# Kernel tuning notes

Hardware: AMD Instinct MI355X
Metric: run time of the kernel (lower is better)

The kernel has to match this reference:

```python
import jax, jax.numpy as jnp
import numpy as np

H = 1536
NH = 24
HD = 64
B = 2
S = 2048


def _rotate_half(x):
    x1, x2 = x[..., : HD // 2], x[..., HD // 2 :]
    return jnp.concatenate((-x2, x1), axis=-1)


def setup_inputs() -> dict:
    key = jax.random.key(0)
    ks = jax.random.split(key, 8)
    scale = 1.0 / np.sqrt(H)
    pos = jnp.arange(S)[:, None]
    inv_freq = 1.0 / (10000.0 ** (jnp.arange(0, HD, 2, dtype=jnp.float32) / HD))
    ang = pos * inv_freq[None, :]
    ang = jnp.concatenate([ang, ang], axis=-1)  # [S, HD]
    return {
        "hidden_states": jax.random.normal(ks[0], (B, S, H), jnp.float32),
        "rope_cos": jnp.cos(ang),
        "rope_sin": jnp.sin(ang),
        "wq": jax.random.normal(ks[1], (H, H), jnp.float32) * scale,
        "bq": jnp.zeros((H,), jnp.float32),
        "wk": jax.random.normal(ks[2], (H, H), jnp.float32) * scale,
        "bk": jnp.zeros((H,), jnp.float32),
        "wv": jax.random.normal(ks[3], (H, H), jnp.float32) * scale,
        "bv": jnp.zeros((H,), jnp.float32),
        "wo": jax.random.normal(ks[4], (H, H), jnp.float32) * scale,
        "bo": jnp.zeros((H,), jnp.float32),
    }


def reference(hidden_states, rope_cos, rope_sin, wq, bq, wk, bk, wv, bv, wo, bo):
    b, s, _ = hidden_states.shape
    # QKV projections (torch Linear: x @ W.T + b)
    q = hidden_states @ wq.T + bq
    k = hidden_states @ wk.T + bk
    v = hidden_states @ wv.T + bv
    # [B, NH, S, HD]
    q = q.reshape(b, s, NH, HD).transpose(0, 2, 1, 3)
    k = k.reshape(b, s, NH, HD).transpose(0, 2, 1, 3)
    v = v.reshape(b, s, NH, HD).transpose(0, 2, 1, 3)
    # RoPE: cos/sin broadcast over batch & heads
    cos = rope_cos[None, None, :, :]
    sin = rope_sin[None, None, :, :]
    q = q * cos + _rotate_half(q) * sin
    k = k * cos + _rotate_half(k) * sin
    # SDPA
    scores = jnp.einsum("bhqd,bhkd->bhqk", q, k) / jnp.sqrt(jnp.float32(HD))
    attn = jax.nn.softmax(scores, axis=-1)
    out = jnp.einsum("bhqk,bhkd->bhqd", attn, v)
    out = out.transpose(0, 2, 1, 3).reshape(b, s, NH * HD)
    return out @ wo.T + bo
```

## Files before the change

### kernel.cpp

```cpp
#include <hip/hip_runtime.h>
#include <hip/hip_bf16.h>
#include <cstdint>

namespace {
constexpr int H_  = 1536;
constexpr int NH_ = 24;
constexpr int HD_ = 64;
constexpr int B_  = 2;
constexpr int S_  = 2048;
constexpr int M_  = B_ * S_;
constexpr int KD_ = H_;
}

typedef __attribute__((ext_vector_type(8))) short  bf16x8;
typedef __attribute__((ext_vector_type(4))) float  f32x4;

__device__ __forceinline__ unsigned short f2bf_fast(float x) {
    return (unsigned short)((__float_as_uint(x) + 0x8000u) >> 16);
}
__device__ __forceinline__ unsigned pack2bf(float b_hi, float a_lo) {
    const unsigned ub = __float_as_uint(b_hi) + 0x8000u;
    const unsigned ua = __float_as_uint(a_lo) + 0x8000u;
    return (ub & 0xffff0000u) | (ua >> 16);
}

__device__ __forceinline__ void gload16(const short* g, short* l) {
    __builtin_amdgcn_global_load_lds(
        (const __attribute__((address_space(1))) unsigned int*)g,
        (__attribute__((address_space(3))) unsigned int*)l, 16, 0, 0);
}

__global__ __launch_bounds__(256)
void cast_all(const float* __restrict__ X,
              const float* __restrict__ wq, const float* __restrict__ wk,
              const float* __restrict__ wv, const float* __restrict__ wo,
              short* __restrict__ Xh,
              short* __restrict__ Wqh, short* __restrict__ Wkh,
              short* __restrict__ Wvh, short* __restrict__ Woh)
{
    constexpr int XB = (M_*H_) / 1024;
    constexpr int WB = (H_*H_) / 1024;
    const int bid = blockIdx.x;
    const float* src; short* dst; int off;
    if (bid < XB)            { src = X;  dst = Xh;  off = bid; }
    else {
        const int r = bid - XB, wsel = r / WB; off = r % WB;
        if      (wsel == 0)  { src = wq; dst = Wqh; }
        else if (wsel == 1)  { src = wk; dst = Wkh; }
        else if (wsel == 2)  { src = wv; dst = Wvh; }
        else                 { src = wo; dst = Woh; }
    }
    const int i = (off * 256 + threadIdx.x) * 4;
    const float4 v = *(const float4*)&src[i];
    uint2 o;
    o.x = pack2bf(v.y, v.x);
    o.y = pack2bf(v.w, v.z);
    *(uint2*)&dst[i] = o;
}

template<int KIND>
__global__ __launch_bounds__(256, 4)
void gemm_bf16(const short* __restrict__ A_g,
               const short* __restrict__ Wq, const short* __restrict__ Wk,
               const short* __restrict__ Wv,
               const float* __restrict__ bq, const float* __restrict__ bk,
               const float* __restrict__ bv,
               const float* __restrict__ cosb, const float* __restrict__ sinb,
               short* __restrict__ Qb, short* __restrict__ Kb,
               short* __restrict__ Vt, float* __restrict__ outf)
{
    __shared__ short Ah[128*64], Bh[128*64];

    const int t    = threadIdx.x;
    const int lane = t & 63;
    const int w    = t >> 6;
    const int wr   = w >> 1, wc = w & 1;
    const int l15  = lane & 15;
    const int grp  = lane >> 4;

    const int xcd = blockIdx.x & 7;
    const int off = blockIdx.x >> 3;
    const int m_idx = xcd * 4 + (off & 3);
    const int rest  = off >> 2;
    const int n_idx = rest % 12;
    const int zi    = (KIND == 0) ? rest / 12 : 3;

    const int m0 = m_idx * 128;
    const int n0 = n_idx * 128;

    const short* bhg; const float* bias;
    if (KIND == 0) {
        if      (zi == 0) { bhg = Wq; bias = bq; }
        else if (zi == 1) { bhg = Wk; bias = bk; }
        else              { bhg = Wv; bias = bv; }
    } else {
        bhg = Wq; bias = bq;
    }

    f32x4 acc[4][4];
#pragma unroll
    for (int i = 0; i < 4; ++i)
#pragma unroll
        for (int j = 0; j < 4; ++j) acc[i][j] = (f32x4){0.f, 0.f, 0.f, 0.f};

    const int srow  = lane >> 3;
    const int sslot = (lane & 7) ^ srow;

    for (int kt = 0; kt < KD_; kt += 64) {
        __syncthreads();
#pragma unroll
        for (int cc = 0; cc < 4; ++cc) {
            const int c = w * 4 + cc;
            const int r = c * 8 + srow;
            gload16(A_g + (size_t)(m0 + r) * KD_ + kt + sslot * 8, Ah + c * 512);
            gload16(bhg + (size_t)(n0 + r) * KD_ + kt + sslot * 8, Bh + c * 512);
        }
        __syncthreads();

#pragma unroll
        for (int kk = 0; kk < 2; ++kk) {
            bf16x8 af[4], bfr[4];
#pragma unroll
            for (int i = 0; i < 4; ++i) {
                const int ra = wr * 64 + i * 16 + l15;
                af[i]  = *(const bf16x8*)&Ah[ra * 64 + (((kk*4 + grp) ^ (ra & 7)) << 3)];
                const int rb = wc * 64 + i * 16 + l15;
                bfr[i] = *(const bf16x8*)&Bh[rb * 64 + (((kk*4 + grp) ^ (rb & 7)) << 3)];
            }
#pragma unroll
            for (int i = 0; i < 4; ++i)
#pragma unroll
                for (int j = 0; j < 4; ++j)
                    acc[i][j] = __builtin_amdgcn_mfma_f32_16x16x32_bf16(af[i], bfr[j], acc[i][j], 0, 0, 0);
        }
    }

    float bn[4];
#pragma unroll
    for (int ni = 0; ni < 4; ++ni) bn[ni] = bias[n0 + wc * 64 + ni * 16 + l15];
    const int hw = (n0 + wc * 64) >> 6;

    if (KIND == 1) {
#pragma unroll
        for (int mi = 0; mi < 4; ++mi)
#pragma unroll
            for (int r = 0; r < 4; ++r) {
                const int m = m0 + wr * 64 + mi * 16 + grp * 4 + r;
#pragma unroll
                for (int ni = 0; ni < 4; ++ni)
                    outf[(size_t)m * H_ + n0 + wc * 64 + ni * 16 + l15] =
                        acc[mi][ni][r] + bn[ni];
            }
        return;
    }

    if (zi == 2) {
        const int b = m0 >> 11;
#pragma unroll
        for (int mi = 0; mi < 4; ++mi) {
            const int sb = (m0 & (S_ - 1)) + wr * 64 + mi * 16 + grp * 4;
#pragma unroll
            for (int ni = 0; ni < 4; ++ni) {
                const int d = ni * 16 + l15;
                uint2 o;
                o.x = pack2bf(acc[mi][ni][1] + bn[ni], acc[mi][ni][0] + bn[ni]);
                o.y = pack2bf(acc[mi][ni][3] + bn[ni], acc[mi][ni][2] + bn[ni]);
                *(uint2*)&Vt[((size_t)(b * NH_ + hw) * HD_ + d) * S_ + sb] = o;
            }
        }
        return;
    }

    const float sc = (zi == 0) ? 0.18033688011112042f : 1.0f;
    short* dst = (zi == 0) ? Qb : Kb;
#pragma unroll
    for (int mi = 0; mi < 4; ++mi)
#pragma unroll
        for (int r = 0; r < 4; ++r) {
            const int m = m0 + wr * 64 + mi * 16 + grp * 4 + r;
            const int b = m >> 11;
            const int s = m & (S_ - 1);
#pragma unroll
            for (int ni = 0; ni < 4; ++ni) {
                const int d  = ni * 16 + l15;
                const float val = acc[mi][ni][r] + bn[ni];
                const float pv  = acc[mi][ni ^ 2][r] + bn[ni ^ 2];
                const float cs = cosb[s * HD_ + d];
                const float sn = sinb[s * HD_ + d];
                const float rot = (ni < 2) ? -pv : pv;
                dst[((size_t)(b * NH_ + hw) * S_ + s) * HD_ + d] =
                    (short)f2bf_fast((val * cs + rot * sn) * sc);
            }
        }
}

__global__ __launch_bounds__(256)
void attn_mfma(const short* __restrict__ Q, const short* __restrict__ K,
               const short* __restrict__ Vt, short* __restrict__ AO)
{
    __shared__ short Ks[2][4096];
    __shared__ short Vs[2][4096];
    __shared__ short Ps[4][1024];

    const int t    = threadIdx.x;
    const int lane = t & 63;
    const int wid  = t >> 6;
    const int bh   = blockIdx.y;
    const int q0   = blockIdx.x * 64;

    const int l15 = lane & 15;
    const int grp = lane >> 4;
    const int sw  = lane & 7;

    const short* Qg = Q  + ((size_t)bh * S_ + q0 + wid*16) * HD_;
    const short* Kg = K  + (size_t)bh * S_ * HD_;
    const short* Vg = Vt + (size_t)bh * HD_ * S_;

    bf16x8 qf[2];
#pragma unroll
    for (int f = 0; f < 2; ++f)
        qf[f] = *(const bf16x8*)(Qg + (size_t)l15*HD_ + f*32 + grp*8);

    f32x4 oacc[4];
#pragma unroll
    for (int nt = 0; nt < 4; ++nt) oacc[nt] = (f32x4){0.f,0.f,0.f,0.f};
    float lacc = 0.f;

    auto stageKV = [&](int b, int kt) {
#pragma unroll
        for (int cc = 0; cc < 2; ++cc) {
            const int d   = cc * 256 + t;
            const int row = d >> 3;
            const int sg  = (d & 7) ^ (row & 7);
            gload16(Kg + (size_t)(kt + row) * HD_ + sg * 8, &Ks[b][d * 8]);
            gload16(Vg + (size_t)row * S_ + kt + sg * 8,    &Vs[b][d * 8]);
        }
    };

    stageKV(0, 0);
    __syncthreads();
    int cur = 0;

    for (int kt = 0; kt < S_; kt += 64) {
        if (kt + 64 < S_) stageKV(cur ^ 1, kt + 64);

        f32x4 sac[4];
#pragma unroll
        for (int nt = 0; nt < 4; ++nt) sac[nt] = (f32x4){0.f,0.f,0.f,0.f};
        __builtin_amdgcn_s_setprio(1);
#pragma unroll
        for (int f = 0; f < 2; ++f) {
            const int slotf = ((grp + f*4) ^ sw) << 3;
#pragma unroll
            for (int nt = 0; nt < 4; ++nt) {
                const bf16x8 kfrag = *(const bf16x8*)&Ks[cur][(nt*16 + l15)*64 + slotf];
                sac[nt] = __builtin_amdgcn_mfma_f32_16x16x32_bf16(kfrag, qf[f], sac[nt], 0, 0, 0);
            }
        }
        __builtin_amdgcn_s_setprio(0);

#pragma unroll
        for (int nt = 0; nt < 4; ++nt)
#pragma unroll
            for (int r = 0; r < 4; ++r) {
                sac[nt][r] = exp2f(sac[nt][r]);
                lacc += sac[nt][r];
            }

#pragma unroll
        for (int nt = 0; nt < 4; ++nt)
#pragma unroll
            for (int rp = 0; rp < 2; ++rp) {
                const int kv0 = nt*16 + grp*4 + rp*2;
                const int idx = l15*64 + (((kv0 >> 3) ^ sw) << 3) + (kv0 & 7);
                *(unsigned*)&Ps[wid][idx] =
                    pack2bf(sac[nt][rp*2+1], sac[nt][rp*2]);
            }

        __builtin_amdgcn_s_setprio(1);
#pragma unroll
        for (int f = 0; f < 2; ++f) {
            const int slotf = ((grp + f*4) ^ sw) << 3;
            const bf16x8 pfrag = *(const bf16x8*)&Ps[wid][l15*64 + slotf];
#pragma unroll
            for (int nt = 0; nt < 4; ++nt) {
                const bf16x8 vfrag = *(const bf16x8*)&Vs[cur][(nt*16 + l15)*64 + slotf];
                oacc[nt] = __builtin_amdgcn_mfma_f32_16x16x32_bf16(vfrag, pfrag, oacc[nt], 0, 0, 0);
            }
        }
        __builtin_amdgcn_s_setprio(0);

        __syncthreads();
        cur ^= 1;
    }

    lacc += __shfl_xor(lacc, 16);
    lacc += __shfl_xor(lacc, 32);
    const float inv = 1.f / lacc;

    const int b = bh / NH_, h = bh % NH_;
    const int srow = q0 + wid*16 + l15;
    const size_t rowb = ((size_t)(b*S_ + srow)) * H_ + h*HD_;
#pragma unroll
    for (int nt = 0; nt < 4; ++nt) {
        uint2 o;
        o.x = pack2bf(oacc[nt][1]*inv, oacc[nt][0]*inv);
        o.y = pack2bf(oacc[nt][3]*inv, oacc[nt][2]*inv);
        *(uint2*)&AO[rowb + nt*16 + grp*4] = o;
    }
}

extern "C" void kernel_launch(void* const* d_in, const int* in_sizes, int n_in,
                              void* d_out, int out_size, void* d_ws, size_t ws_size,
                              hipStream_t stream)
{
    const float* X    = (const float*)d_in[0];
    const float* cosb = (const float*)d_in[1];
    const float* sinb = (const float*)d_in[2];
    const float* wq   = (const float*)d_in[3];
    const float* bq   = (const float*)d_in[4];
    const float* wk   = (const float*)d_in[5];
    const float* bk   = (const float*)d_in[6];
    const float* wv   = (const float*)d_in[7];
    const float* bv   = (const float*)d_in[8];
    const float* wo   = (const float*)d_in[9];
    const float* bo   = (const float*)d_in[10];
    float* out = (float*)d_out;

    const size_t MH = (size_t)M_ * H_;
    const size_t HH = (size_t)H_ * H_;

    short* Xh  = (short*)d_ws;
    short* Wqh = Xh  + MH;
    short* Wkh = Wqh + HH;
    short* Wvh = Wkh + HH;
    short* Woh = Wvh + HH;
    short* Qb  = Woh + HH;
    short* Kb  = Qb + MH;
    short* Vt  = Kb + MH;
    short* AO  = Vt + MH;

    cast_all<<<(int)(MH/1024 + 4*(HH/1024)), 256, 0, stream>>>(
        X, wq, wk, wv, wo, Xh, Wqh, Wkh, Wvh, Woh);

    gemm_bf16<0><<<1152, 256, 0, stream>>>(Xh, Wqh, Wkh, Wvh,
        bq, bk, bv, cosb, sinb, Qb, Kb, Vt, nullptr);

    attn_mfma<<<dim3(S_/64, B_*NH_), 256, 0, stream>>>(Qb, Kb, Vt, AO);

    gemm_bf16<1><<<384, 256, 0, stream>>>(AO, Woh, nullptr, nullptr,
        bo, nullptr, nullptr, nullptr, nullptr, nullptr, nullptr, nullptr, out);
}
```

Measured before the change: 225.4 us.

## Switch attention to 32x32x16 MFMA with 128-row query tiles per block

The attention kernel now uses 32x32x16 bf16 MFMA, and each wave handles 32 query rows instead of 16, so a block covers 128 queries. Each K/V tile staged in LDS is reused across twice as many queries, which halves global K/V traffic and LDS fragment reads per query row. Launch bounds request 3 blocks per SM. The cost is more registers per wave (16-wide accumulators), a larger P buffer in LDS, half as many blocks (768), and more complex scattered output stores.

```diff
diff --git a/kernel.cpp b/kernel.cpp
--- a/kernel.cpp
+++ b/kernel.cpp
@@ -12,8 +12,9 @@
 constexpr int KD_ = H_;
 }
 
-typedef __attribute__((ext_vector_type(8))) short  bf16x8;
-typedef __attribute__((ext_vector_type(4))) float  f32x4;
+typedef __attribute__((ext_vector_type(8)))  short bf16x8;
+typedef __attribute__((ext_vector_type(4)))  float f32x4;
+typedef __attribute__((ext_vector_type(16))) float f32x16;
 
 __device__ __forceinline__ unsigned short f2bf_fast(float x) {
     return (unsigned short)((__float_as_uint(x) + 0x8000u) >> 16);
@@ -194,36 +195,38 @@
         }
 }
 
-__global__ __launch_bounds__(256)
+__global__ __launch_bounds__(256, 3)
 void attn_mfma(const short* __restrict__ Q, const short* __restrict__ K,
                const short* __restrict__ Vt, short* __restrict__ AO)
 {
     __shared__ short Ks[2][4096];
     __shared__ short Vs[2][4096];
-    __shared__ short Ps[4][1024];
+    __shared__ short Ps[4][2048];
 
     const int t    = threadIdx.x;
     const int lane = t & 63;
     const int wid  = t >> 6;
     const int bh   = blockIdx.y;
-    const int q0   = blockIdx.x * 64;
-
-    const int l15 = lane & 15;
-    const int grp = lane >> 4;
-    const int sw  = lane & 7;
-
-    const short* Qg = Q  + ((size_t)bh * S_ + q0 + wid*16) * HD_;
+    const int q0   = blockIdx.x * 128;
+
+    const int l31 = lane & 31;
+    const int hi  = lane >> 5;
+    const int sw7 = lane & 7;
+
+    const short* Qg = Q  + ((size_t)bh * S_ + q0 + wid*32) * HD_;
     const short* Kg = K  + (size_t)bh * S_ * HD_;
     const short* Vg = Vt + (size_t)bh * HD_ * S_;
 
-    bf16x8 qf[2];
-#pragma unroll
-    for (int f = 0; f < 2; ++f)
-        qf[f] = *(const bf16x8*)(Qg + (size_t)l15*HD_ + f*32 + grp*8);
-
-    f32x4 oacc[4];
-#pragma unroll
-    for (int nt = 0; nt < 4; ++nt) oacc[nt] = (f32x4){0.f,0.f,0.f,0.f};
+    bf16x8 qf[4];
+#pragma unroll
+    for (int kk = 0; kk < 4; ++kk)
+        qf[kk] = *(const bf16x8*)(Qg + (size_t)l31*HD_ + kk*16 + hi*8);
+
+    f32x16 oacc[2];
+#pragma unroll
+    for (int nt = 0; nt < 2; ++nt)
+#pragma unroll
+        for (int r = 0; r < 16; ++r) oacc[nt][r] = 0.f;
     float lacc = 0.f;
 
     auto stageKV = [&](int b, int kt) {
@@ -244,48 +247,53 @@
     for (int kt = 0; kt < S_; kt += 64) {
         if (kt + 64 < S_) stageKV(cur ^ 1, kt + 64);
 
-        f32x4 sac[4];
-#pragma unroll
-        for (int nt = 0; nt < 4; ++nt) sac[nt] = (f32x4){0.f,0.f,0.f,0.f};
+        f32x16 sac[2];
+#pragma unroll
+        for (int nt = 0; nt < 2; ++nt)
+#pragma unroll
+            for (int r = 0; r < 16; ++r) sac[nt][r] = 0.f;
         __builtin_amdgcn_s_setprio(1);
 #pragma unroll
-        for (int f = 0; f < 2; ++f) {
-            const int slotf = ((grp + f*4) ^ sw) << 3;
-#pragma unroll
-            for (int nt = 0; nt < 4; ++nt) {
-                const bf16x8 kfrag = *(const bf16x8*)&Ks[cur][(nt*16 + l15)*64 + slotf];
-                sac[nt] = __builtin_amdgcn_mfma_f32_16x16x32_bf16(kfrag, qf[f], sac[nt], 0, 0, 0);
+        for (int kk = 0; kk < 4; ++kk) {
+#pragma unroll
+            for (int nt = 0; nt < 2; ++nt) {
+                const int row = nt*32 + l31;
+                const bf16x8 kfrag = *(const bf16x8*)
+                    &Ks[cur][row*64 + (((kk*2 + hi) ^ sw7) << 3)];
+                sac[nt] = __builtin_amdgcn_mfma_f32_32x32x16_bf16(kfrag, qf[kk], sac[nt], 0, 0, 0);
             }
         }
         __builtin_amdgcn_s_setprio(0);
 
 #pragma unroll
-        for (int nt = 0; nt < 4; ++nt)
-#pragma unroll
-            for (int r = 0; r < 4; ++r) {
+        for (int nt = 0; nt < 2; ++nt)
+#pragma unroll
+            for (int r = 0; r < 16; ++r) {
                 sac[nt][r] = exp2f(sac[nt][r]);
                 lacc += sac[nt][r];
             }
 
 #pragma unroll
-        for (int nt = 0; nt < 4; ++nt)
-#pragma unroll
-            for (int rp = 0; rp < 2; ++rp) {
-                const int kv0 = nt*16 + grp*4 + rp*2;
-                const int idx = l15*64 + (((kv0 >> 3) ^ sw) << 3) + (kv0 & 7);
-                *(unsigned*)&Ps[wid][idx] =
-                    pack2bf(sac[nt][rp*2+1], sac[nt][rp*2]);
+        for (int h = 0; h < 2; ++h)
+#pragma unroll
+            for (int i = 0; i < 8; ++i) {
+                const int crow = ((2*i) & 3) + 8*((2*i) >> 2) + 4*hi;
+                const int kv   = h*32 + crow;
+                const int idx  = l31*64 + ((((kv >> 3) ^ sw7)) << 3) + (kv & 7);
+                *(unsigned*)&Ps[wid][idx] = pack2bf(sac[h][2*i+1], sac[h][2*i]);
             }
 
         __builtin_amdgcn_s_setprio(1);
 #pragma unroll
-        for (int f = 0; f < 2; ++f) {
-            const int slotf = ((grp + f*4) ^ sw) << 3;
-            const bf16x8 pfrag = *(const bf16x8*)&Ps[wid][l15*64 + slotf];
-#pragma unroll
-            for (int nt = 0; nt < 4; ++nt) {
-                const bf16x8 vfrag = *(const bf16x8*)&Vs[cur][(nt*16 + l15)*64 + slotf];
-                oacc[nt] = __builtin_amdgcn_mfma_f32_16x16x32_bf16(vfrag, pfrag, oacc[nt], 0, 0, 0);
+        for (int ks = 0; ks < 4; ++ks) {
+            const bf16x8 pfrag = *(const bf16x8*)
+                &Ps[wid][l31*64 + (((ks*2 + hi) ^ sw7) << 3)];
+#pragma unroll
+            for (int nt = 0; nt < 2; ++nt) {
+                const int row = nt*32 + l31;
+                const bf16x8 vfrag = *(const bf16x8*)
+                    &Vs[cur][row*64 + (((ks*2 + hi) ^ sw7) << 3)];
+                oacc[nt] = __builtin_amdgcn_mfma_f32_32x32x16_bf16(vfrag, pfrag, oacc[nt], 0, 0, 0);
             }
         }
         __builtin_amdgcn_s_setprio(0);
@@ -294,20 +302,21 @@
         cur ^= 1;
     }
 
-    lacc += __shfl_xor(lacc, 16);
     lacc += __shfl_xor(lacc, 32);
     const float inv = 1.f / lacc;
 
     const int b = bh / NH_, h = bh % NH_;
-    const int srow = q0 + wid*16 + l15;
+    const int srow = q0 + wid*32 + l31;
     const size_t rowb = ((size_t)(b*S_ + srow)) * H_ + h*HD_;
 #pragma unroll
-    for (int nt = 0; nt < 4; ++nt) {
-        uint2 o;
-        o.x = pack2bf(oacc[nt][1]*inv, oacc[nt][0]*inv);
-        o.y = pack2bf(oacc[nt][3]*inv, oacc[nt][2]*inv);
-        *(uint2*)&AO[rowb + nt*16 + grp*4] = o;
-    }
+    for (int nt = 0; nt < 2; ++nt)
+#pragma unroll
+        for (int i = 0; i < 8; ++i) {
+            const int crow = ((2*i) & 3) + 8*((2*i) >> 2) + 4*hi;
+            const int d    = nt*32 + crow;
+            *(unsigned*)&AO[rowb + d] =
+                pack2bf(oacc[nt][2*i+1]*inv, oacc[nt][2*i]*inv);
+        }
 }
 
 extern "C" void kernel_launch(void* const* d_in, const int* in_sizes, int n_in,
@@ -346,7 +355,7 @@
     gemm_bf16<0><<<1152, 256, 0, stream>>>(Xh, Wqh, Wkh, Wvh,
         bq, bk, bv, cosb, sinb, Qb, Kb, Vt, nullptr);
 
-    attn_mfma<<<dim3(S_/64, B_*NH_), 256, 0, stream>>>(Qb, Kb, Vt, AO);
+    attn_mfma<<<dim3(S_/128, B_*NH_), 256, 0, stream>>>(Qb, Kb, Vt, AO);
 
     gemm_bf16<1><<<384, 256, 0, stream>>>(AO, Woh, nullptr, nullptr,
         bo, nullptr, nullptr, nullptr, nullptr, nullptr, nullptr, nullptr, out);
```

After: 214.5 us. 4.8% less time.
